# Performance work log

Measured on AMD Instinct MI355X. Metric: run time of the kernel, lower is better.

## Reference

```python
import jax, jax.numpy as jnp
import numpy as np
import math

E = 500_000   # edges
N = 2_000     # nodes (small so duplicate (src,dst) pairs form real groups)
D = 128       # embedding_dim == n_heads*qkv_dim
H = 8         # heads
DK = 16       # qkv_dim
HH = 256      # hyper hidden
EMBD = 2      # hyper embd_dim
CLIP = 10.0   # tanh_clipping


def setup_inputs() -> dict:
    key = jax.random.key(0)
    ks = jax.random.split(key, 12)
    # shared_nodes: inverse indices of unique edge (src,dst) columns (reset() preprocessing)
    rng = np.random.default_rng(0)
    edge_indices = rng.integers(0, N, size=(2, E))
    _, inv = np.unique(edge_indices, axis=1, return_inverse=True)
    shared_nodes = jnp.asarray(inv.reshape(-1), dtype=jnp.int32)

    def lin(k, shape, fan_in):
        return jax.random.normal(k, shape, jnp.float32) / np.sqrt(fan_in)

    return {
        "pref": jax.random.uniform(ks[0], (2,), jnp.float32),
        "dists": jax.random.uniform(ks[1], (E, 2), jnp.float32),
        "edge_emb": jax.random.normal(ks[2], (E, D), jnp.float32),
        "shared_nodes": shared_nodes,
        "fc1_w": lin(ks[3], (HH, 2), 2), "fc1_b": jnp.zeros((HH,), jnp.float32),
        "fc2_w": lin(ks[4], (HH, HH), HH), "fc2_b": jnp.zeros((HH,), jnp.float32),
        "fc3_w": lin(ks[5], (2 * EMBD, HH), HH), "fc3_b": jnp.zeros((2 * EMBD,), jnp.float32),
        "wq_w": lin(ks[6], (D * H * DK, EMBD), EMBD),
        "wk_w": lin(ks[7], (D * H * DK, EMBD), EMBD),
    }


def reference(pref, dists, edge_emb, shared_nodes,
              fc1_w, fc1_b, fc2_w, fc2_b, fc3_w, fc3_b, wq_w, wk_w):
    # --- assign(pref): hypernetwork producing Wq, Wk (no activations, per source) ---
    h = pref @ fc1_w.T + fc1_b
    h = h @ fc2_w.T + fc2_b
    mid = h @ fc3_w.T + fc3_b                    # [4]
    Wq = (mid[:EMBD] @ wq_w.T).reshape(D, H * DK)
    Wk = (mid[EMBD:2 * EMBD] @ wk_w.T).reshape(D, H * DK)

    # --- reset(): scalarized distances + group means over shared edge groups ---
    d = pref[0] * dists[:, 0] + pref[1] * dists[:, 1]   # [E]
    n_edges = edge_emb.shape[0]
    seg = shared_nodes
    group_sums = jax.ops.segment_sum(edge_emb, seg, num_segments=n_edges)
    counts = jax.ops.segment_sum(jnp.ones((n_edges,), edge_emb.dtype), seg,
                                 num_segments=n_edges)
    group_means = group_sums / jnp.clip(counts, 1.0)[:, None]
    q = group_means[seg]                          # [E, D]

    # --- forward(): edge-wise multi-head dot score, tanh clip, group softmax ---
    fq = (q @ Wq.T).reshape(n_edges, H, DK)       # F.linear(q, Wq) (D == H*DK)
    fk = (edge_emb @ Wk.T).reshape(n_edges, H, DK)
    score = (fq * fk).sum(-1).mean(-1) / math.sqrt(D) - d / math.sqrt(2.0)
    score = CLIP * jnp.tanh(score)

    seg_max = jax.ops.segment_max(score, seg, num_segments=n_edges)
    ex = jnp.exp(score - seg_max[seg])
    denom = jax.ops.segment_sum(ex, seg, num_segments=n_edges)
    probs = ex / denom[seg]
    return probs[:, None]                         # [E, 1]
```

## Files before the change

### kernel.cpp

```cpp
#include <hip/hip_runtime.h>
#include <math.h>

#define DD 128
#define HHID 256
#define SLOTS 8

__global__ void k_setup(const float* __restrict__ pref,
                        const float* __restrict__ fc1_w, const float* __restrict__ fc1_b,
                        const float* __restrict__ fc2_w, const float* __restrict__ fc2_b,
                        const float* __restrict__ fc3_w, const float* __restrict__ fc3_b,
                        const float* __restrict__ wq_w, const float* __restrict__ wk_w,
                        const int* __restrict__ seg, unsigned* __restrict__ counts,
                        float* __restrict__ M_, int E_) {
    if (blockIdx.x >= 64) {
        int e = (int)(blockIdx.x - 64) * blockDim.x + threadIdx.x;
        if (e < E_) atomicAdd(&counts[seg[e]], 1u);
        return;
    }
    __shared__ float h1[HHID];
    __shared__ float h2[HHID];
    __shared__ float mid[4];
    int t = threadIdx.x;
    float p0 = pref[0], p1 = pref[1];
    h1[t] = fc1_w[t * 2 + 0] * p0 + fc1_w[t * 2 + 1] * p1 + fc1_b[t];
    __syncthreads();
    float acc = fc2_b[t];
    for (int i = 0; i < HHID; ++i) acc += fc2_w[t * HHID + i] * h1[i];
    h2[t] = acc;
    __syncthreads();
    if (t < 4) {
        float m = fc3_b[t];
        for (int i = 0; i < HHID; ++i) m += fc3_w[t * HHID + i] * h2[i];
        mid[t] = m;
    }
    __syncthreads();
    float m0 = mid[0], m1 = mid[1], m2 = mid[2], m3 = mid[3];
    int r = blockIdx.x * 2 + (t >> 7);
    int c = t & 127;
    const float scale = 0.011048543456f;
    float s = 0.f;
    for (int a = 0; a < DD; ++a) {
        float wq = wq_w[(a * DD + r) * 2 + 0] * m0 + wq_w[(a * DD + r) * 2 + 1] * m1;
        float wk = wk_w[(a * DD + c) * 2 + 0] * m2 + wk_w[(a * DD + c) * 2 + 1] * m3;
        s += wq * wk;
    }
    M_[r * DD + c] = s * scale;
}

__global__ void k_classify(const int* __restrict__ seg, const unsigned* __restrict__ counts,
                           unsigned* __restrict__ slot, int* __restrict__ mem,
                           int* __restrict__ glist, int* __restrict__ nctr,
                           float* __restrict__ out, int E_) {
    __shared__ int lcnt;
    __shared__ int lbase;
    int tid = blockIdx.x * blockDim.x + threadIdx.x;
    if (threadIdx.x == 0) lcnt = 0;
    __syncthreads();
    bool claim = false;
    int lpos = 0;
    if (tid < E_) {
        int g = seg[tid];
        unsigned c = counts[g];
        if (c == 1u) {
            out[tid] = 1.0f;
        } else {
            unsigned j = atomicAdd(&slot[g], 1u);
            if (j < SLOTS) mem[(size_t)g * SLOTS + j] = tid;
        }
        claim = (counts[tid] >= 2u);
        if (claim) lpos = atomicAdd(&lcnt, 1);
    }
    __syncthreads();
    if (threadIdx.x == 0 && lcnt) lbase = atomicAdd(&nctr[1], lcnt);
    __syncthreads();
    if (claim) glist[lbase + lpos] = tid;
}

__global__ __launch_bounds__(256) void k_fused(const int* __restrict__ glist,
                                               const int* __restrict__ nctr,
                                               const unsigned* __restrict__ counts,
                                               const int* __restrict__ mem,
                                               const float4* __restrict__ M4,
                                               const float4* __restrict__ emb4,
                                               const float2* __restrict__ emb2,
                                               const float2* __restrict__ dists2,
                                               const float* __restrict__ pref,
                                               float* __restrict__ out) {
    __shared__ float meanT[DD * 32];
    __shared__ float gtile[32 * DD];
    int t = threadIdx.x;
    int ng = nctr[1];
    int ntile = (ng + 31) >> 5;
    float p0 = pref[0], p1 = pref[1];
    for (int tile = blockIdx.x; tile < ntile; tile += gridDim.x) {
        int i0 = tile * 32;
        {
            int gi = t & 31;
            int kq = t >> 5;
            int i = i0 + gi;
            float4 s0 = make_float4(0.f, 0.f, 0.f, 0.f), s1 = s0, s2 = s0, s3 = s0;
            float inv = 0.f;
            if (i < ng) {
                int g = glist[i];
                unsigned c = counts[g];
                int cm = (int)(c < (unsigned)SLOTS ? c : (unsigned)SLOTS);
                inv = 1.0f / (float)c;
                for (int j = 0; j < cm; ++j) {
                    int e = mem[(size_t)g * SLOTS + j];
                    float4 v0 = emb4[(size_t)e * 32 + kq + 0];
                    float4 v1 = emb4[(size_t)e * 32 + kq + 8];
                    float4 v2 = emb4[(size_t)e * 32 + kq + 16];
                    float4 v3 = emb4[(size_t)e * 32 + kq + 24];
                    s0.x += v0.x; s0.y += v0.y; s0.z += v0.z; s0.w += v0.w;
                    s1.x += v1.x; s1.y += v1.y; s1.z += v1.z; s1.w += v1.w;
                    s2.x += v2.x; s2.y += v2.y; s2.z += v2.z; s2.w += v2.w;
                    s3.x += v3.x; s3.y += v3.y; s3.z += v3.z; s3.w += v3.w;
                }
            }
            int k0 = (kq + 0) * 4, k1 = (kq + 8) * 4, k2 = (kq + 16) * 4, k3 = (kq + 24) * 4;
            meanT[(k0 + 0) * 32 + gi] = s0.x * inv; meanT[(k0 + 1) * 32 + gi] = s0.y * inv;
            meanT[(k0 + 2) * 32 + gi] = s0.z * inv; meanT[(k0 + 3) * 32 + gi] = s0.w * inv;
            meanT[(k1 + 0) * 32 + gi] = s1.x * inv; meanT[(k1 + 1) * 32 + gi] = s1.y * inv;
            meanT[(k1 + 2) * 32 + gi] = s1.z * inv; meanT[(k1 + 3) * 32 + gi] = s1.w * inv;
            meanT[(k2 + 0) * 32 + gi] = s2.x * inv; meanT[(k2 + 1) * 32 + gi] = s2.y * inv;
            meanT[(k2 + 2) * 32 + gi] = s2.z * inv; meanT[(k2 + 3) * 32 + gi] = s2.w * inv;
            meanT[(k3 + 0) * 32 + gi] = s3.x * inv; meanT[(k3 + 1) * 32 + gi] = s3.y * inv;
            meanT[(k3 + 2) * 32 + gi] = s3.z * inv; meanT[(k3 + 3) * 32 + gi] = s3.w * inv;
        }
        __syncthreads();
        {
            int cseg = t & 31;
            int g4 = (t >> 5) * 4;
            float4 acc0 = make_float4(0.f, 0.f, 0.f, 0.f);
            float4 acc1 = acc0, acc2 = acc0, acc3 = acc0;
            #pragma unroll 4
            for (int k = 0; k < DD; ++k) {
                float4 mv = *(const float4*)&meanT[k * 32 + g4];
                float4 Mr = M4[k * 32 + cseg];
                acc0.x += mv.x * Mr.x; acc0.y += mv.x * Mr.y; acc0.z += mv.x * Mr.z; acc0.w += mv.x * Mr.w;
                acc1.x += mv.y * Mr.x; acc1.y += mv.y * Mr.y; acc1.z += mv.y * Mr.z; acc1.w += mv.y * Mr.w;
                acc2.x += mv.z * Mr.x; acc2.y += mv.z * Mr.y; acc2.z += mv.z * Mr.z; acc2.w += mv.z * Mr.w;
                acc3.x += mv.w * Mr.x; acc3.y += mv.w * Mr.y; acc3.z += mv.w * Mr.z; acc3.w += mv.w * Mr.w;
            }
            *(float4*)&gtile[(g4 + 0) * DD + cseg * 4] = acc0;
            *(float4*)&gtile[(g4 + 1) * DD + cseg * 4] = acc1;
            *(float4*)&gtile[(g4 + 2) * DD + cseg * 4] = acc2;
            *(float4*)&gtile[(g4 + 3) * DD + cseg * 4] = acc3;
        }
        __syncthreads();
        {
            int w = t >> 6;
            int lane = t & 63;
            for (int q = 0; q < 8; ++q) {
                int gl = w * 8 + q;
                int i = i0 + gl;
                if (i >= ng) continue;
                int g = glist[i];
                unsigned c = counts[g];
                int cm = (int)(c < (unsigned)SLOTS ? c : (unsigned)SLOTS);
                float2 tv = *(const float2*)&gtile[gl * DD + 2 * lane];
                float s_mine = 0.f;
                for (int j = 0; j < cm; ++j) {
                    int e = mem[(size_t)g * SLOTS + j];
                    float2 kv = emb2[(size_t)e * 64 + lane];
                    float d = tv.x * kv.x + tv.y * kv.y;
                    for (int off = 32; off; off >>= 1) d += __shfl_xor(d, off, 64);
                    if (lane == j) s_mine = d;
                }
                int e_lane = -1;
                if (lane < cm) {
                    e_lane = mem[(size_t)g * SLOTS + lane];
                    float2 dd = dists2[e_lane];
                    float de = p0 * dd.x + p1 * dd.y;
                    s_mine = 10.0f * tanhf(s_mine - de * 0.7071067811865475f);
                }
                float v = (lane < cm) ? s_mine : -3.0e38f;
                for (int off = 32; off; off >>= 1) v = fmaxf(v, __shfl_xor(v, off, 64));
                float ex = (lane < cm) ? __expf(s_mine - v) : 0.f;
                float sm = ex;
                for (int off = 32; off; off >>= 1) sm += __shfl_xor(sm, off, 64);
                if (lane < cm) out[e_lane] = ex / sm;
            }
        }
        __syncthreads();
    }
}

extern "C" void kernel_launch(void* const* d_in, const int* in_sizes, int n_in,
                              void* d_out, int out_size, void* d_ws, size_t ws_size,
                              hipStream_t stream) {
    const float* pref  = (const float*)d_in[0];
    const float* dists = (const float*)d_in[1];
    const float* emb   = (const float*)d_in[2];
    const int*   seg   = (const int*)d_in[3];
    const float* fc1_w = (const float*)d_in[4];
    const float* fc1_b = (const float*)d_in[5];
    const float* fc2_w = (const float*)d_in[6];
    const float* fc2_b = (const float*)d_in[7];
    const float* fc3_w = (const float*)d_in[8];
    const float* fc3_b = (const float*)d_in[9];
    const float* wq_w  = (const float*)d_in[10];
    const float* wk_w  = (const float*)d_in[11];
    int E_ = in_sizes[3];
    float* out = (float*)d_out;

    char* ws = (char*)d_ws;
    int*      nctr   = (int*)ws;
    unsigned* counts = (unsigned*)(ws + 256);
    unsigned* slot   = (unsigned*)(ws + 256 + (size_t)E_ * 4);
    size_t zero_bytes = 256 + (size_t)E_ * 8;
    char* p = ws + ((zero_bytes + 255) & ~(size_t)255);
    int*   glist = (int*)p;   p += ((size_t)E_ * 4 + 255) & ~(size_t)255;
    float* M_    = (float*)p; p += (size_t)DD * DD * 4;
    int*   mem   = (int*)p;   p += (size_t)E_ * SLOTS * 4;
    if ((size_t)(p - ws) > ws_size) return;

    hipMemsetAsync(ws, 0, zero_bytes, stream);

    int tb = 256;
    int eb = (E_ + tb - 1) / tb;
    k_setup<<<64 + eb, tb, 0, stream>>>(pref, fc1_w, fc1_b, fc2_w, fc2_b, fc3_w, fc3_b,
                                        wq_w, wk_w, seg, counts, M_, E_);
    k_classify<<<eb, tb, 0, stream>>>(seg, counts, slot, mem, glist, nctr, out, E_);
    k_fused<<<1024, 256, 0, stream>>>(glist, nctr, counts, mem, (const float4*)M_,
                                      (const float4*)emb, (const float2*)emb,
                                      (const float2*)dists, pref, out);
}
```

Baseline: 439.1 us.

## Pack counts and slots into one word, vectorize edge passes, cache Wq row

```diff
diff --git a/kernel.cpp b/kernel.cpp
--- a/kernel.cpp
+++ b/kernel.cpp
@@ -4,22 +4,32 @@
 #define DD 128
 #define HHID 256
 #define SLOTS 8
+
 
 __global__ void k_setup(const float* __restrict__ pref,
                         const float* __restrict__ fc1_w, const float* __restrict__ fc1_b,
                         const float* __restrict__ fc2_w, const float* __restrict__ fc2_b,
                         const float* __restrict__ fc3_w, const float* __restrict__ fc3_b,
                         const float* __restrict__ wq_w, const float* __restrict__ wk_w,
-                        const int* __restrict__ seg, unsigned* __restrict__ counts,
+                        const int* __restrict__ seg, unsigned* __restrict__ cs,
                         float* __restrict__ M_, int E_) {
     if (blockIdx.x >= 64) {
-        int e = (int)(blockIdx.x - 64) * blockDim.x + threadIdx.x;
-        if (e < E_) atomicAdd(&counts[seg[e]], 1u);
+        int base = ((int)(blockIdx.x - 64) * blockDim.x + threadIdx.x) * 4;
+        if (base + 3 < E_) {
+            int4 s4 = *(const int4*)&seg[base];
+            atomicAdd(&cs[s4.x], 1u);
+            atomicAdd(&cs[s4.y], 1u);
+            atomicAdd(&cs[s4.z], 1u);
+            atomicAdd(&cs[s4.w], 1u);
+        } else {
+            for (int e = base; e < E_; ++e) atomicAdd(&cs[seg[e]], 1u);
+        }
         return;
     }
     __shared__ float h1[HHID];
     __shared__ float h2[HHID];
     __shared__ float mid[4];
+    __shared__ float wqv[2 * DD];
     int t = threadIdx.x;
     float p0 = pref[0], p1 = pref[1];
     h1[t] = fc1_w[t * 2 + 0] * p0 + fc1_w[t * 2 + 1] * p1 + fc1_b[t];
@@ -35,50 +45,74 @@
     }
     __syncthreads();
     float m0 = mid[0], m1 = mid[1], m2 = mid[2], m3 = mid[3];
-    int r = blockIdx.x * 2 + (t >> 7);
+    {
+        int a = t & 127, rh = t >> 7;
+        int r = blockIdx.x * 2 + rh;
+        wqv[rh * DD + a] = wq_w[(a * DD + r) * 2 + 0] * m0 + wq_w[(a * DD + r) * 2 + 1] * m1;
+    }
+    __syncthreads();
+    int rh = t >> 7;
+    int r = blockIdx.x * 2 + rh;
     int c = t & 127;
     const float scale = 0.011048543456f;
     float s = 0.f;
     for (int a = 0; a < DD; ++a) {
-        float wq = wq_w[(a * DD + r) * 2 + 0] * m0 + wq_w[(a * DD + r) * 2 + 1] * m1;
         float wk = wk_w[(a * DD + c) * 2 + 0] * m2 + wk_w[(a * DD + c) * 2 + 1] * m3;
-        s += wq * wk;
+        s += wqv[rh * DD + a] * wk;
     }
     M_[r * DD + c] = s * scale;
 }
 
-__global__ void k_classify(const int* __restrict__ seg, const unsigned* __restrict__ counts,
-                           unsigned* __restrict__ slot, int* __restrict__ mem,
-                           int* __restrict__ glist, int* __restrict__ nctr,
-                           float* __restrict__ out, int E_) {
+__global__ void k_classify(const int* __restrict__ seg, unsigned* __restrict__ cs,
+                           int* __restrict__ mem, int* __restrict__ glist,
+                           int* __restrict__ nctr, float* __restrict__ out, int E_) {
     __shared__ int lcnt;
     __shared__ int lbase;
-    int tid = blockIdx.x * blockDim.x + threadIdx.x;
-    if (threadIdx.x == 0) lcnt = 0;
-    __syncthreads();
-    bool claim = false;
+    int t = threadIdx.x;
+    if (t == 0) lcnt = 0;
+    __syncthreads();
+    int base = (blockIdx.x * blockDim.x + t) * 4;
+#define EDGE_STEP(K, G) { unsigned c = cs[(G)] & 0xffffu;                         \
+        if (c == 1u) { out[base + (K)] = 1.0f; }                                  \
+        else { unsigned old = atomicAdd(&cs[(G)], 0x10000u);                      \
+               unsigned j = old >> 16;                                            \
+               if (j < SLOTS) mem[(size_t)(G) * SLOTS + j] = base + (K); } }
+    if (base + 3 < E_) {
+        int4 s4 = *(const int4*)&seg[base];
+        EDGE_STEP(0, s4.x) EDGE_STEP(1, s4.y) EDGE_STEP(2, s4.z) EDGE_STEP(3, s4.w)
+    } else {
+        for (int e = base; e < E_; ++e) {
+            int g = seg[e];
+            unsigned c = cs[g] & 0xffffu;
+            if (c == 1u) { out[e] = 1.0f; }
+            else { unsigned old = atomicAdd(&cs[g], 0x10000u);
+                   unsigned j = old >> 16;
+                   if (j < SLOTS) mem[(size_t)g * SLOTS + j] = e; }
+        }
+    }
+#undef EDGE_STEP
+    bool c0 = (base + 0 < E_) && (cs[base + 0] & 0xffffu) >= 2u;
+    bool c1 = (base + 1 < E_) && (cs[base + 1] & 0xffffu) >= 2u;
+    bool c2 = (base + 2 < E_) && (cs[base + 2] & 0xffffu) >= 2u;
+    bool c3 = (base + 3 < E_) && (cs[base + 3] & 0xffffu) >= 2u;
+    int m = (int)c0 + (int)c1 + (int)c2 + (int)c3;
     int lpos = 0;
-    if (tid < E_) {
-        int g = seg[tid];
-        unsigned c = counts[g];
-        if (c == 1u) {
-            out[tid] = 1.0f;
-        } else {
-            unsigned j = atomicAdd(&slot[g], 1u);
-            if (j < SLOTS) mem[(size_t)g * SLOTS + j] = tid;
-        }
-        claim = (counts[tid] >= 2u);
-        if (claim) lpos = atomicAdd(&lcnt, 1);
-    }
-    __syncthreads();
-    if (threadIdx.x == 0 && lcnt) lbase = atomicAdd(&nctr[1], lcnt);
-    __syncthreads();
-    if (claim) glist[lbase + lpos] = tid;
+    if (m) lpos = atomicAdd(&lcnt, m);
+    __syncthreads();
+    if (t == 0 && lcnt) lbase = atomicAdd(&nctr[1], lcnt);
+    __syncthreads();
+    if (m) {
+        int p = lbase + lpos;
+        if (c0) glist[p++] = base + 0;
+        if (c1) glist[p++] = base + 1;
+        if (c2) glist[p++] = base + 2;
+        if (c3) glist[p++] = base + 3;
+    }
 }
 
 __global__ __launch_bounds__(256) void k_fused(const int* __restrict__ glist,
                                                const int* __restrict__ nctr,
-                                               const unsigned* __restrict__ counts,
+                                               const unsigned* __restrict__ cs,
                                                const int* __restrict__ mem,
                                                const float4* __restrict__ M4,
                                                const float4* __restrict__ emb4,
@@ -102,7 +136,7 @@
             float inv = 0.f;
             if (i < ng) {
                 int g = glist[i];
-                unsigned c = counts[g];
+                unsigned c = cs[g] & 0xffffu;
                 int cm = (int)(c < (unsigned)SLOTS ? c : (unsigned)SLOTS);
                 inv = 1.0f / (float)c;
                 for (int j = 0; j < cm; ++j) {
@@ -156,20 +190,19 @@
                 int i = i0 + gl;
                 if (i >= ng) continue;
                 int g = glist[i];
-                unsigned c = counts[g];
+                unsigned c = cs[g] & 0xffffu;
                 int cm = (int)(c < (unsigned)SLOTS ? c : (unsigned)SLOTS);
+                int e_lane = (lane < cm) ? mem[(size_t)g * SLOTS + lane] : 0;
                 float2 tv = *(const float2*)&gtile[gl * DD + 2 * lane];
                 float s_mine = 0.f;
                 for (int j = 0; j < cm; ++j) {
-                    int e = mem[(size_t)g * SLOTS + j];
+                    int e = __shfl(e_lane, j, 64);
                     float2 kv = emb2[(size_t)e * 64 + lane];
                     float d = tv.x * kv.x + tv.y * kv.y;
                     for (int off = 32; off; off >>= 1) d += __shfl_xor(d, off, 64);
                     if (lane == j) s_mine = d;
                 }
-                int e_lane = -1;
                 if (lane < cm) {
-                    e_lane = mem[(size_t)g * SLOTS + lane];
                     float2 dd = dists2[e_lane];
                     float de = p0 * dd.x + p1 * dd.y;
                     s_mine = 10.0f * tanhf(s_mine - de * 0.7071067811865475f);
@@ -205,10 +238,9 @@
     float* out = (float*)d_out;
 
     char* ws = (char*)d_ws;
-    int*      nctr   = (int*)ws;
-    unsigned* counts = (unsigned*)(ws + 256);
-    unsigned* slot   = (unsigned*)(ws + 256 + (size_t)E_ * 4);
-    size_t zero_bytes = 256 + (size_t)E_ * 8;
+    int*      nctr = (int*)ws;
+    unsigned* cs   = (unsigned*)(ws + 256);
+    size_t zero_bytes = 256 + (size_t)E_ * 4;
     char* p = ws + ((zero_bytes + 255) & ~(size_t)255);
     int*   glist = (int*)p;   p += ((size_t)E_ * 4 + 255) & ~(size_t)255;
     float* M_    = (float*)p; p += (size_t)DD * DD * 4;
@@ -218,11 +250,11 @@
     hipMemsetAsync(ws, 0, zero_bytes, stream);
 
     int tb = 256;
-    int eb = (E_ + tb - 1) / tb;
-    k_setup<<<64 + eb, tb, 0, stream>>>(pref, fc1_w, fc1_b, fc2_w, fc2_b, fc3_w, fc3_b,
-                                        wq_w, wk_w, seg, counts, M_, E_);
-    k_classify<<<eb, tb, 0, stream>>>(seg, counts, slot, mem, glist, nctr, out, E_);
-    k_fused<<<1024, 256, 0, stream>>>(glist, nctr, counts, mem, (const float4*)M_,
+    int eb4 = (E_ + tb * 4 - 1) / (tb * 4);
+    k_setup<<<64 + eb4, tb, 0, stream>>>(pref, fc1_w, fc1_b, fc2_w, fc2_b, fc3_w, fc3_b,
+                                         wq_w, wk_w, seg, cs, M_, E_);
+    k_classify<<<eb4, tb, 0, stream>>>(seg, cs, mem, glist, nctr, out, E_);
+    k_fused<<<1024, 256, 0, stream>>>(glist, nctr, cs, mem, (const float4*)M_,
                                       (const float4*)emb, (const float2*)emb,
                                       (const float2*)dists, pref, out);
 }
```

Measured after the change: 420.9 us. -4.1%, faster.
